# Kernel tuning notes

Measured on AMD Instinct MI355X. Metric: run time of the kernel, lower is better.

The kernel has to match this reference:

```python
import jax, jax.numpy as jnp
import numpy as np

B, S, D, FF, H, N, P, K, KP, R = 2, 512, 256, 1024, 4, 512, 32, 16, 4, 64
DH = D // H  # 64


def _ln(x, g, b):
    mu = x.mean(-1, keepdims=True)
    var = ((x - mu) ** 2).mean(-1, keepdims=True)
    return (x - mu) * jax.lax.rsqrt(var + 1e-5) * g + b


def setup_inputs() -> dict:
    key = jax.random.key(0)
    ks = iter(jax.random.split(key, 40))
    nrm = lambda shape, std=0.02: jax.random.normal(next(ks), shape, jnp.float32) * std
    return dict(
        x=jax.random.normal(next(ks), (B, S, D), jnp.float32),
        g1=jnp.ones((D,), jnp.float32), b1=jnp.zeros((D,), jnp.float32),
        g2=jnp.ones((D,), jnp.float32), b2=jnp.zeros((D,), jnp.float32),
        Wq=nrm((D, D)), bq=jnp.zeros((D,), jnp.float32),
        Wk=nrm((D, D)), bk=jnp.zeros((D,), jnp.float32),
        Wv=nrm((D, D)), bv=jnp.zeros((D,), jnp.float32),
        Wpath=nrm((2 * D, 2)), bpath=jnp.zeros((2,), jnp.float32),
        neurons=nrm((N, D)),
        Wnq=nrm((D, D)), bnq=jnp.zeros((D,), jnp.float32),
        Wnk=nrm((D, D)), bnk=jnp.zeros((D,), jnp.float32),
        Wnv=nrm((D, D)), bnv=jnp.zeros((D,), jnp.float32),
        pattern_queries=nrm((P, D)),
        pattern_up_A=nrm((P, D, R)),
        pattern_up_B=nrm((P, R, FF), 0.01),
        Wub=nrm((D, FF), 0.01), bub=jnp.zeros((FF,), jnp.float32),
        Wd=nrm((FF, D), 0.02), bd=jnp.zeros((D,), jnp.float32),
    )


def _forward(x, g1, b1, g2, b2, Wq, bq, Wk, bk, Wv, bv, Wpath, bpath, neurons,
             Wnq, bnq, Wnk, bnk, Wnv, bnv, pattern_queries, pattern_up_A,
             pattern_up_B, Wub, bub, Wd, bd):
    # ---- NeuronRouter on norm1(x) ----
    n1 = _ln(x, g1, b1)
    q = (n1 @ Wq + bq).reshape(B, S, H, DH)
    k = (n1 @ Wk + bk).reshape(B, S, H, DH)
    v = (n1 @ Wv + bv).reshape(B, S, H, DH)
    attn = jax.nn.softmax(jnp.einsum('bqhd,bkhd->bhqk', q, k) / np.float32(np.sqrt(DH)), axis=-1)
    context = jnp.einsum('bhqk,bkhd->bqhd', attn, v).reshape(B, S, D)
    token_scores = n1 @ neurons.T        # [B,S,N]
    context_scores = context @ neurons.T
    w = jax.nn.softmax(jnp.concatenate([n1, context], -1) @ Wpath + bpath, axis=-1)
    scores = w[..., 0:1] * token_scores + w[..., 1:2] * context_scores
    topk_scores, topk_idx = jax.lax.top_k(scores, K)
    topk_w = jax.nn.softmax(topk_scores, axis=-1)      # [B,S,K]
    selected = neurons[topk_idx]                        # [B,S,K,D]

    # ---- InteractionFFN on norm2(x) ----
    n2 = _ln(x, g2, b2)
    qn = (selected @ Wnq + bnq).reshape(B, S, K, H, DH)
    kn = (selected @ Wnk + bnk).reshape(B, S, K, H, DH)
    vn = jax.nn.sigmoid((selected @ Wnv + bnv).reshape(B, S, K, H, DH))
    aw = jax.nn.softmax(jnp.einsum('bsqhd,bskhd->bshqk', qn, kn) / np.float32(np.sqrt(DH)), axis=-1)
    gates = jnp.einsum('bshqk,bskhd->bsqhd', aw, vn).reshape(B, S, K, D)
    aggregated = jnp.sum(topk_w[..., None] * (selected * gates), axis=2)  # [B,S,D]

    pattern_scores = 0.5 * (aggregated @ pattern_queries.T) / np.float32(np.sqrt(D)) \
                     + 0.5 * (context @ pattern_queries.T)               # [B,S,P]
    tps, tpi = jax.lax.top_k(pattern_scores, KP)
    tpw = jax.nn.softmax(tps, axis=-1)                                   # [B,S,KP]

    combined = n2 + aggregated
    A = pattern_up_A[tpi]    # [B,S,KP,D,R]  (gathered per-token LoRA A)
    Bm = pattern_up_B[tpi]   # [B,S,KP,R,FF] (gathered per-token LoRA B)
    h_mid = jnp.einsum('bsd,bskdr->bskr', combined, A)
    h_pat = jnp.einsum('bskr,bskrf->bskf', h_mid, Bm)
    h_pattern = jnp.sum(tpw[..., None] * h_pat, axis=2)                  # [B,S,FF]
    h = jax.nn.gelu(0.1 * (combined @ Wub + bub) + 0.9 * h_pattern, approximate=False)
    out = h @ Wd + bd
    return x + out, topk_idx


def reference(x, g1, b1, g2, b2, Wq, bq, Wk, bk, Wv, bv, Wpath, bpath, neurons,
              Wnq, bnq, Wnk, bnk, Wnv, bnv, pattern_queries, pattern_up_A,
              pattern_up_B, Wub, bub, Wd, bd):
    return _forward(x, g1, b1, g2, b2, Wq, bq, Wk, bk, Wv, bv, Wpath, bpath,
                    neurons, Wnq, bnq, Wnk, bnk, Wnv, bnv, pattern_queries,
                    pattern_up_A, pattern_up_B, Wub, bub, Wd, bd)
```

## Files before the change

### kernel.cpp

```cpp
#include <hip/hip_runtime.h>
#include <hip/hip_bf16.h>
#include <math.h>

#define BB 2
#define SS 512
#define DD 256
#define FFD 1024
#define HH 4
#define NN 512
#define PP 32
#define KK 16
#define KPP 4
#define RR 64
#define DHH 64
#define TT (BB*SS)
#define QT 16

__global__ __launch_bounds__(256) void ln_kernel(
    const float* __restrict__ x,
    const float* __restrict__ g1, const float* __restrict__ b1,
    const float* __restrict__ g2, const float* __restrict__ b2,
    float* __restrict__ n1, float* __restrict__ n2)
{
    int t = blockIdx.x;
    int d = threadIdx.x;
    __shared__ float red[256];
    float v = x[t*DD + d];
    red[d] = v; __syncthreads();
    for (int s = 128; s > 0; s >>= 1) { if (d < s) red[d] += red[d+s]; __syncthreads(); }
    float mu = red[0] * (1.0f/DD);
    __syncthreads();
    float dv = v - mu;
    red[d] = dv*dv; __syncthreads();
    for (int s = 128; s > 0; s >>= 1) { if (d < s) red[d] += red[d+s]; __syncthreads(); }
    float var = red[0] * (1.0f/DD);
    float r = 1.0f / sqrtf(var + 1e-5f);
    n1[t*DD+d] = dv*r*g1[d] + b1[d];
    n2[t*DD+d] = dv*r*g2[d] + b2[d];
}

__device__ __forceinline__ void gemm_body(
    const float* __restrict__ A, const float* __restrict__ Bm,
    const float* __restrict__ bias, const float* __restrict__ extra,
    float* __restrict__ C, int M, int Nn, int Kk, int transB, int mode,
    int k0off, int kLen)
{
    __shared__ float As[2][32][68];
    __shared__ float Bs[2][32][68];
    int bm = blockIdx.y * 64;
    int bn = blockIdx.x * 64;
    int tid = threadIdx.x;
    int tx = tid & 15, ty = tid >> 4;

    float4 pa[2], pb[2];

    #define LOAD_A(kbase) { \
        _Pragma("unroll") \
        for (int e = 0; e < 2; ++e) { \
            int r = e*32 + (tid>>3); int c4 = tid & 7; \
            pa[e] = *(const float4*)&A[(size_t)(bm + r)*Kk + (kbase) + c4*4]; \
        } }
    #define STORE_A(buf) { \
        _Pragma("unroll") \
        for (int e = 0; e < 2; ++e) { \
            int r = e*32 + (tid>>3); int c4 = tid & 7; \
            As[buf][c4*4+0][r] = pa[e].x; \
            As[buf][c4*4+1][r] = pa[e].y; \
            As[buf][c4*4+2][r] = pa[e].z; \
            As[buf][c4*4+3][r] = pa[e].w; \
        } }
    #define LOAD_B(kbase) { \
        if (transB == 0) { \
            _Pragma("unroll") \
            for (int e = 0; e < 2; ++e) { \
                int c = e*16 + (tid>>4); int n4 = tid & 15; \
                pb[e] = *(const float4*)&Bm[(size_t)((kbase) + c)*Nn + bn + n4*4]; \
            } \
        } else { \
            _Pragma("unroll") \
            for (int e = 0; e < 2; ++e) { \
                int r = e*32 + (tid>>3); int k4 = tid & 7; \
                pb[e] = *(const float4*)&Bm[(size_t)(bn + r)*Kk + (kbase) + k4*4]; \
            } \
        } }
    #define STORE_B(buf) { \
        if (transB == 0) { \
            _Pragma("unroll") \
            for (int e = 0; e < 2; ++e) { \
                int c = e*16 + (tid>>4); int n4 = tid & 15; \
                *(float4*)&Bs[buf][c][n4*4] = pb[e]; \
            } \
        } else { \
            _Pragma("unroll") \
            for (int e = 0; e < 2; ++e) { \
                int r = e*32 + (tid>>3); int k4 = tid & 7; \
                Bs[buf][k4*4+0][r] = pb[e].x; \
                Bs[buf][k4*4+1][r] = pb[e].y; \
                Bs[buf][k4*4+2][r] = pb[e].z; \
                Bs[buf][k4*4+3][r] = pb[e].w; \
            } \
        } }

    float acc[4][4] = {};
    int nk = kLen >> 5;

    LOAD_A(k0off); LOAD_B(k0off);
    STORE_A(0); STORE_B(0);
    __syncthreads();

    for (int kt = 0; kt < nk; ++kt) {
        int cur = kt & 1;
        if (kt + 1 < nk) { LOAD_A(k0off + (kt+1)*32); LOAD_B(k0off + (kt+1)*32); }
        #pragma unroll
        for (int kk = 0; kk < 32; ++kk) {
            float4 av = *(const float4*)&As[cur][kk][ty*4];
            float4 bv = *(const float4*)&Bs[cur][kk][tx*4];
            acc[0][0] = fmaf(av.x, bv.x, acc[0][0]);
            acc[0][1] = fmaf(av.x, bv.y, acc[0][1]);
            acc[0][2] = fmaf(av.x, bv.z, acc[0][2]);
            acc[0][3] = fmaf(av.x, bv.w, acc[0][3]);
            acc[1][0] = fmaf(av.y, bv.x, acc[1][0]);
            acc[1][1] = fmaf(av.y, bv.y, acc[1][1]);
            acc[1][2] = fmaf(av.y, bv.z, acc[1][2]);
            acc[1][3] = fmaf(av.y, bv.w, acc[1][3]);
            acc[2][0] = fmaf(av.z, bv.x, acc[2][0]);
            acc[2][1] = fmaf(av.z, bv.y, acc[2][1]);
            acc[2][2] = fmaf(av.z, bv.z, acc[2][2]);
            acc[2][3] = fmaf(av.z, bv.w, acc[2][3]);
            acc[3][0] = fmaf(av.w, bv.x, acc[3][0]);
            acc[3][1] = fmaf(av.w, bv.y, acc[3][1]);
            acc[3][2] = fmaf(av.w, bv.z, acc[3][2]);
            acc[3][3] = fmaf(av.w, bv.w, acc[3][3]);
        }
        if (kt + 1 < nk) {
            STORE_A(cur^1); STORE_B(cur^1);
            __syncthreads();
        }
    }

    #pragma unroll
    for (int i = 0; i < 4; ++i) {
        int m = bm + ty*4 + i;
        #pragma unroll
        for (int j = 0; j < 4; ++j) {
            int n = bn + tx*4 + j;
            float val = acc[i][j] + (bias ? bias[n] : 0.0f);
            if (mode == 1) {
                val = 1.0f / (1.0f + expf(-val));
            } else if (mode == 2) {
                float z = 0.1f*val + 0.9f*extra[(size_t)m*Nn+n];
                val = 0.5f*z*(1.0f + erff(z*0.70710678118654752f));
            } else if (mode == 3) {
                val = val + extra[(size_t)m*Nn+n];
            }
            C[(size_t)m*Nn + n] = val;
        }
    }
    #undef LOAD_A
    #undef STORE_A
    #undef LOAD_B
    #undef STORE_B
}

__global__ __launch_bounds__(256) void gemm_kernel(
    const float* __restrict__ A, const float* __restrict__ Bm,
    const float* __restrict__ bias, const float* __restrict__ extra,
    float* __restrict__ C, int M, int Nn, int Kk, int transB, int mode)
{
    gemm_body(A, Bm, bias, extra, C, M, Nn, Kk, transB, mode, 0, Kk);
}

struct GemmSet { const float* A; const float* B; const float* bias; float* C; int mode; };

__global__ __launch_bounds__(256) void gemm3_kernel(
    GemmSet s0, GemmSet s1, GemmSet s2, int M, int Nn, int Kk, int transB)
{
    GemmSet s = (blockIdx.z == 0) ? s0 : ((blockIdx.z == 1) ? s1 : s2);
    gemm_body(s.A, s.B, s.bias, nullptr, s.C, M, Nn, Kk, transB, s.mode, 0, Kk);
}

__global__ __launch_bounds__(256) void gemm_splitk_kernel(
    const float* __restrict__ A, const float* __restrict__ Bm,
    float* __restrict__ Cpart, int M, int Nn, int Kk, int kPerSplit)
{
    int sk = blockIdx.z;
    float* Cp = Cpart + (size_t)sk * M * Nn;
    gemm_body(A, Bm, nullptr, nullptr, Cp, M, Nn, Kk, 0, 0, sk*kPerSplit, kPerSplit);
}

__global__ __launch_bounds__(256) void combine_wd_kernel(
    const float* __restrict__ part, const float* __restrict__ x,
    const float* __restrict__ bd, float* __restrict__ out)
{
    int i = blockIdx.x*256 + threadIdx.x;
    int d = i & (DD-1);
    float s = x[i] + bd[d];
    s += part[i] + part[i + TT*DD] + part[i + 2*TT*DD] + part[i + 3*TT*DD];
    out[i] = s;
}

__global__ __launch_bounds__(256) void attn_kernel(
    const float* __restrict__ q, const float* __restrict__ k,
    const float* __restrict__ v, float* __restrict__ ctx)
{
    int bi = blockIdx.x;
    int qt = bi & 31;
    int bh = bi >> 5;
    int h = bh & (HH-1);
    int b = bh >> 2;
    int tid = threadIdx.x;
    int qo = tid >> 4;
    int c  = tid & 15;

    __shared__ float Qs[QT][68];
    __shared__ float Kt[64][64];
    __shared__ float Vs[64][68];
    __shared__ float Ps[QT][68];

    {
        const float* qp = q + ((size_t)(b*SS + qt*QT + qo)*DD) + h*DHH + c*4;
        *(float4*)&Qs[qo][c*4] = *(const float4*)qp;
    }
    float O0=0.f, O1=0.f, O2=0.f, O3=0.f;
    float mreg = -3.4e38f, lreg = 0.f;

    for (int t = 0; t < 8; ++t) {
        if (t) __syncthreads();
        #pragma unroll
        for (int e = 0; e < 4; ++e) {
            int lin = e*256 + tid;
            int kr = lin & 63;
            int c4 = lin >> 6;
            const float* kp = k + ((size_t)(b*SS + t*64 + kr)*DD) + h*DHH + c4*4;
            float4 kv = *(const float4*)kp;
            Kt[c4*4+0][kr] = kv.x;
            Kt[c4*4+1][kr] = kv.y;
            Kt[c4*4+2][kr] = kv.z;
            Kt[c4*4+3][kr] = kv.w;
            int vr = lin >> 4;
            int vc = lin & 15;
            const float* vp = v + ((size_t)(b*SS + t*64 + vr)*DD) + h*DHH + vc*4;
            *(float4*)&Vs[vr][vc*4] = *(const float4*)vp;
        }
        __syncthreads();
        float s0=0.f, s1=0.f, s2=0.f, s3=0.f;
        #pragma unroll 8
        for (int d = 0; d < 64; ++d) {
            float qv = Qs[qo][d];
            float4 kv = *(const float4*)&Kt[d][c*4];
            s0 = fmaf(qv, kv.x, s0);
            s1 = fmaf(qv, kv.y, s1);
            s2 = fmaf(qv, kv.z, s2);
            s3 = fmaf(qv, kv.w, s3);
        }
        s0 *= 0.125f; s1 *= 0.125f; s2 *= 0.125f; s3 *= 0.125f;
        float mx = fmaxf(fmaxf(s0, s1), fmaxf(s2, s3));
        #pragma unroll
        for (int mk = 1; mk <= 8; mk <<= 1)
            mx = fmaxf(mx, __shfl_xor(mx, mk));
        float mnew = fmaxf(mreg, mx);
        float scl = __expf(mreg - mnew);
        float e0 = __expf(s0 - mnew), e1 = __expf(s1 - mnew),
              e2 = __expf(s2 - mnew), e3 = __expf(s3 - mnew);
        float esum = e0 + e1 + e2 + e3;
        #pragma unroll
        for (int mk = 1; mk <= 8; mk <<= 1)
            esum += __shfl_xor(esum, mk);
        lreg = lreg * scl + esum;
        mreg = mnew;
        float4 pw; pw.x = e0; pw.y = e1; pw.z = e2; pw.w = e3;
        *(float4*)&Ps[qo][c*4] = pw;
        __syncthreads();
        O0 *= scl; O1 *= scl; O2 *= scl; O3 *= scl;
        #pragma unroll 8
        for (int kk = 0; kk < 64; ++kk) {
            float pv = Ps[qo][kk];
            float4 vv = *(const float4*)&Vs[kk][c*4];
            O0 = fmaf(pv, vv.x, O0);
            O1 = fmaf(pv, vv.y, O1);
            O2 = fmaf(pv, vv.z, O2);
            O3 = fmaf(pv, vv.w, O3);
        }
    }
    float linv = 1.0f / lreg;
    float4 o4; o4.x = O0*linv; o4.y = O1*linv; o4.z = O2*linv; o4.w = O3*linv;
    *(float4*)(ctx + ((size_t)(b*SS + qt*QT + qo)*DD) + h*DHH + c*4) = o4;
}

__global__ __launch_bounds__(256) void route_kernel(
    const float* __restrict__ n1, const float* __restrict__ ctx,
    const float* __restrict__ Wpath, const float* __restrict__ bpath,
    const float* __restrict__ ts, const float* __restrict__ cs,
    int* __restrict__ topk_idx, float* __restrict__ topk_w,
    float* __restrict__ out_idx)
{
    int t = blockIdx.x, tid = threadIdx.x;
    __shared__ float red0[256], red1[256];
    float a = n1[t*DD+tid], c = ctx[t*DD+tid];
    red0[tid] = a * Wpath[tid*2+0] + c * Wpath[(DD+tid)*2+0];
    red1[tid] = a * Wpath[tid*2+1] + c * Wpath[(DD+tid)*2+1];
    __syncthreads();
    for (int s = 128; s > 0; s >>= 1) {
        if (tid < s) { red0[tid] += red0[tid+s]; red1[tid] += red1[tid+s]; }
        __syncthreads();
    }
    __shared__ float w0s, w1s;
    if (tid == 0) {
        float l0 = red0[0] + bpath[0], l1 = red1[0] + bpath[1];
        float mm = fmaxf(l0, l1);
        float e0 = expf(l0-mm), e1 = expf(l1-mm);
        float is = 1.0f/(e0+e1);
        w0s = e0*is; w1s = e1*is;
    }
    __syncthreads();
    float w0 = w0s, w1 = w1s;
    __shared__ float sc[NN];
    sc[tid]     = w0*ts[t*NN+tid]     + w1*cs[t*NN+tid];
    sc[tid+256] = w0*ts[t*NN+tid+256] + w1*cs[t*NN+tid+256];
    __syncthreads();
    __shared__ float bv_[256]; __shared__ int bi_[256];
    __shared__ float selv[KK]; __shared__ int seli[KK];
    for (int it = 0; it < KK; ++it) {
        float v0 = sc[tid], v1 = sc[tid+256];
        float bv; int bi;
        if (v0 >= v1) { bv = v0; bi = tid; } else { bv = v1; bi = tid+256; }
        bv_[tid] = bv; bi_[tid] = bi;
        __syncthreads();
        for (int s = 128; s > 0; s >>= 1) {
            if (tid < s) {
                float ov = bv_[tid+s]; int oi = bi_[tid+s];
                if (ov > bv_[tid] || (ov == bv_[tid] && oi < bi_[tid])) { bv_[tid] = ov; bi_[tid] = oi; }
            }
            __syncthreads();
        }
        if (tid == 0) { selv[it] = bv_[0]; seli[it] = bi_[0]; sc[bi_[0]] = -3.4e38f; }
        __syncthreads();
    }
    if (tid == 0) {
        float mx = selv[0];
        float e[KK]; float sum = 0.f;
        for (int i = 0; i < KK; ++i) { e[i] = expf(selv[i]-mx); sum += e[i]; }
        float is = 1.0f/sum;
        for (int i = 0; i < KK; ++i) {
            topk_idx[t*KK+i] = seli[i];
            topk_w[t*KK+i]   = e[i]*is;
            out_idx[t*KK+i]  = (float)seli[i];
        }
    }
}

__global__ __launch_bounds__(256) void interact_kernel(
    const float* __restrict__ neurons,
    const float* __restrict__ nqa, const float* __restrict__ nka,
    const float* __restrict__ nva,
    const int* __restrict__ topk_idx, const float* __restrict__ topk_w,
    float* __restrict__ agg)
{
    int t = blockIdx.x, tid = threadIdx.x;
    __shared__ float nq[KK][DD+1];
    __shared__ float nk[KK][DD+1];
    __shared__ float nv[KK][DD+1];
    __shared__ float ps[HH][KK][KK];
    __shared__ float tw[KK];
    __shared__ int sidx[KK];
    if (tid < KK) { tw[tid] = topk_w[t*KK+tid]; sidx[tid] = topk_idx[t*KK+tid]; }
    __syncthreads();
    for (int i = 0; i < KK; ++i) {
        int idx = sidx[i];
        nq[i][tid] = nqa[idx*DD+tid];
        nk[i][tid] = nka[idx*DD+tid];
        nv[i][tid] = nva[idx*DD+tid];
    }
    __syncthreads();
    #pragma unroll
    for (int r = 0; r < 4; ++r) {
        int lin = r*256 + tid;
        int j = lin & 15, i = (lin >> 4) & 15, h = lin >> 8;
        const float* qp = &nq[i][h*DHH];
        const float* kp = &nk[j][h*DHH];
        float acc = 0.f;
        #pragma unroll 8
        for (int d = 0; d < DHH; ++d) acc = fmaf(qp[d], kp[d], acc);
        ps[h][i][j] = acc * 0.125f;
    }
    __syncthreads();
    if (tid < 64) {
        int h = tid >> 4, i = tid & 15;
        float mx = -3.4e38f;
        for (int j = 0; j < KK; ++j) mx = fmaxf(mx, ps[h][i][j]);
        float sum = 0.f;
        for (int j = 0; j < KK; ++j) { float e = expf(ps[h][i][j]-mx); ps[h][i][j] = e; sum += e; }
        float is = 1.0f/sum;
        for (int j = 0; j < KK; ++j) ps[h][i][j] *= is;
    }
    __syncthreads();
    int d = tid, h = d >> 6;
    float acc = 0.f;
    for (int i = 0; i < KK; ++i) {
        float g = 0.f;
        #pragma unroll
        for (int j = 0; j < KK; ++j) g = fmaf(ps[h][i][j], nv[j][d], g);
        acc += tw[i] * neurons[sidx[i]*DD + d] * g;
    }
    agg[t*DD+d] = acc;
}

__global__ __launch_bounds__(256) void pattern_kernel(
    const float* __restrict__ aggp, const float* __restrict__ ctxp,
    const float* __restrict__ n2p, const float* __restrict__ PQ,
    const float* __restrict__ Aup, const float* __restrict__ Bup,
    float* __restrict__ combined, float* __restrict__ hpat)
{
    int t = blockIdx.x, tid = threadIdx.x;
    __shared__ float mix[DD], comb[DD];
    __shared__ float ps[PP];
    __shared__ float psp[8][33];
    __shared__ float hmid[KPP][RR];
    __shared__ int tpi[KPP];
    __shared__ float tpw[KPP];

    float a = aggp[t*DD+tid];
    float cx = ctxp[t*DD+tid];
    mix[tid] = 0.03125f * a + 0.5f * cx;
    float cb = n2p[t*DD+tid] + a;
    comb[tid] = cb;
    combined[t*DD+tid] = cb;
    __syncthreads();

    {
        int p = tid & 31, g = tid >> 5;
        const float* pq = PQ + p*DD + g*32;
        const float* mp = mix + g*32;
        float acc = 0.f;
        #pragma unroll
        for (int d = 0; d < 32; ++d) acc = fmaf(mp[d], pq[d], acc);
        psp[g][p] = acc;
    }
    __syncthreads();
    if (tid < PP) {
        float s = 0.f;
        #pragma unroll
        for (int g = 0; g < 8; ++g) s += psp[g][tid];
        ps[tid] = s;
    }
    __syncthreads();

    if (tid == 0) {
        float vals[KPP];
        #pragma unroll
        for (int it = 0; it < KPP; ++it) {
            float bv = -3.4e38f; int bi = 0;
            for (int p = 0; p < PP; ++p) { float v = ps[p]; if (v > bv) { bv = v; bi = p; } }
            vals[it] = bv; tpi[it] = bi; ps[bi] = -3.4e38f;
        }
        float mx = vals[0];
        float e0 = expf(vals[0]-mx), e1 = expf(vals[1]-mx),
              e2 = expf(vals[2]-mx), e3 = expf(vals[3]-mx);
        float is = 1.0f/(e0+e1+e2+e3);
        tpw[0]=e0*is; tpw[1]=e1*is; tpw[2]=e2*is; tpw[3]=e3*is;
    }
    __syncthreads();

    {
        int kp = tid >> 6, r = tid & 63;
        const float* Ap = Aup + (size_t)tpi[kp]*(DD*RR) + r;
        float acc = 0.f;
        #pragma unroll 8
        for (int d = 0; d < DD; ++d) acc = fmaf(comb[d], Ap[(size_t)d*RR], acc);
        hmid[kp][r] = acc * tpw[kp];
    }
    __syncthreads();

    {
        float4 acc = make_float4(0.f, 0.f, 0.f, 0.f);
        #pragma unroll
        for (int kp = 0; kp < KPP; ++kp) {
            const float4* Bp = (const float4*)(Bup + (size_t)tpi[kp]*(RR*FFD)) + tid;
            const float* hm = hmid[kp];
            #pragma unroll 8
            for (int r = 0; r < RR; ++r) {
                float4 b = Bp[(size_t)r*(FFD/4)];
                float h = hm[r];
                acc.x = fmaf(h, b.x, acc.x);
                acc.y = fmaf(h, b.y, acc.y);
                acc.z = fmaf(h, b.z, acc.z);
                acc.w = fmaf(h, b.w, acc.w);
            }
        }
        ((float4*)(hpat + (size_t)t*FFD))[tid] = acc;
    }
}

extern "C" void kernel_launch(void* const* d_in, const int* in_sizes, int n_in,
                              void* d_out, int out_size, void* d_ws, size_t ws_size,
                              hipStream_t stream)
{
    const float* x        = (const float*)d_in[0];
    const float* g1       = (const float*)d_in[1];
    const float* b1       = (const float*)d_in[2];
    const float* g2       = (const float*)d_in[3];
    const float* b2       = (const float*)d_in[4];
    const float* Wq       = (const float*)d_in[5];
    const float* bq       = (const float*)d_in[6];
    const float* Wk       = (const float*)d_in[7];
    const float* bk       = (const float*)d_in[8];
    const float* Wv       = (const float*)d_in[9];
    const float* bv       = (const float*)d_in[10];
    const float* Wpath    = (const float*)d_in[11];
    const float* bpath    = (const float*)d_in[12];
    const float* neurons  = (const float*)d_in[13];
    const float* Wnq      = (const float*)d_in[14];
    const float* bnq      = (const float*)d_in[15];
    const float* Wnk      = (const float*)d_in[16];
    const float* bnk      = (const float*)d_in[17];
    const float* Wnv      = (const float*)d_in[18];
    const float* bnv      = (const float*)d_in[19];
    const float* PQ       = (const float*)d_in[20];
    const float* Aup      = (const float*)d_in[21];
    const float* Bup      = (const float*)d_in[22];
    const float* Wub      = (const float*)d_in[23];
    const float* bub      = (const float*)d_in[24];
    const float* Wd       = (const float*)d_in[25];
    const float* bd       = (const float*)d_in[26];

    float* out0    = (float*)d_out;
    float* out_idx = out0 + (size_t)TT*DD;

    float* ws = (float*)d_ws;
    float* n1   = ws; ws += TT*DD;
    float* n2   = ws; ws += TT*DD;
    float* qb   = ws; ws += TT*DD;
    float* kb   = ws; ws += TT*DD;
    float* vb   = ws; ws += TT*DD;
    float* ctx  = ws; ws += TT*DD;
    float* ts   = ws; ws += TT*NN;
    float* cs   = ws; ws += TT*NN;
    float* nqa  = ws; ws += NN*DD;
    float* nka  = ws; ws += NN*DD;
    float* nva  = ws; ws += NN*DD;
    float* agg  = ws; ws += TT*DD;
    float* comb = ws; ws += TT*DD;
    float* hpat = ws; ws += TT*FFD;
    float* hb   = ws; ws += TT*FFD;
    float* part = ws; ws += 4*TT*DD;
    float* tkw  = ws; ws += TT*KK;
    int*   tki  = (int*)ws; ws += TT*KK;

    dim3 blk(256);

    ln_kernel<<<TT, blk, 0, stream>>>(x, g1, b1, g2, b2, n1, n2);

    {
        GemmSet sq{n1, Wq, bq, qb, 0}, sk{n1, Wk, bk, kb, 0}, sv{n1, Wv, bv, vb, 0};
        gemm3_kernel<<<dim3(DD/64, TT/64, 3), blk, 0, stream>>>(sq, sk, sv, TT, DD, DD, 0);
    }

    {
        GemmSet s0{neurons, Wnq, bnq, nqa, 0}, s1{neurons, Wnk, bnk, nka, 0},
                s2{neurons, Wnv, bnv, nva, 1};
        gemm3_kernel<<<dim3(DD/64, NN/64, 3), blk, 0, stream>>>(s0, s1, s2, NN, DD, DD, 0);
    }

    attn_kernel<<<BB*HH*(SS/QT), blk, 0, stream>>>(qb, kb, vb, ctx);

    {
        GemmSet s0{n1, neurons, nullptr, ts, 0}, s1{ctx, neurons, nullptr, cs, 0};
        gemm3_kernel<<<dim3(NN/64, TT/64, 2), blk, 0, stream>>>(s0, s1, s1, TT, NN, DD, 1);
    }

    route_kernel<<<TT, blk, 0, stream>>>(n1, ctx, Wpath, bpath, ts, cs, tki, tkw, out_idx);

    interact_kernel<<<TT, blk, 0, stream>>>(neurons, nqa, nka, nva, tki, tkw, agg);

    pattern_kernel<<<TT, blk, 0, stream>>>(agg, ctx, n2, PQ, Aup, Bup, comb, hpat);

    gemm_kernel<<<dim3(FFD/64, TT/64), blk, 0, stream>>>(comb, Wub, bub, hpat, hb, TT, FFD, DD, 0, 2);

    gemm_splitk_kernel<<<dim3(DD/64, TT/64, 4), blk, 0, stream>>>(hb, Wd, part, TT, DD, FFD, FFD/4);
    combine_wd_kernel<<<TT*DD/256, blk, 0, stream>>>(part, x, bd, out0);
}
```

Measured before the change: 318.9 us.

## Bin tokens by selected pattern to reuse LoRA weights across tokens

```diff
diff --git a/kernel.cpp b/kernel.cpp
--- a/kernel.cpp
+++ b/kernel.cpp
@@ -15,6 +15,12 @@
 #define DHH 64
 #define TT (BB*SS)
 #define QT 16
+
+__global__ __launch_bounds__(64) void zero_kernel(int* __restrict__ p, int n)
+{
+    int i = threadIdx.x;
+    if (i < n) p[i] = 0;
+}
 
 __global__ __launch_bounds__(256) void ln_kernel(
     const float* __restrict__ x,
@@ -148,7 +154,10 @@
             if (mode == 1) {
                 val = 1.0f / (1.0f + expf(-val));
             } else if (mode == 2) {
-                float z = 0.1f*val + 0.9f*extra[(size_t)m*Nn+n];
+                size_t idx = (size_t)m*Nn + n;
+                float hp = extra[idx] + extra[idx + (size_t)TT*FFD]
+                         + extra[idx + 2*(size_t)TT*FFD] + extra[idx + 3*(size_t)TT*FFD];
+                float z = 0.1f*val + 0.9f*hp;
                 val = 0.5f*z*(1.0f + erff(z*0.70710678118654752f));
             } else if (mode == 3) {
                 val = val + extra[(size_t)m*Nn+n];
@@ -295,18 +304,22 @@
     float* __restrict__ out_idx)
 {
     int t = blockIdx.x, tid = threadIdx.x;
-    __shared__ float red0[256], red1[256];
+    int wv = tid >> 6;
+    __shared__ float pw0[4], pw1[4];
     float a = n1[t*DD+tid], c = ctx[t*DD+tid];
-    red0[tid] = a * Wpath[tid*2+0] + c * Wpath[(DD+tid)*2+0];
-    red1[tid] = a * Wpath[tid*2+1] + c * Wpath[(DD+tid)*2+1];
-    __syncthreads();
-    for (int s = 128; s > 0; s >>= 1) {
-        if (tid < s) { red0[tid] += red0[tid+s]; red1[tid] += red1[tid+s]; }
-        __syncthreads();
-    }
+    float r0 = a * Wpath[tid*2+0] + c * Wpath[(DD+tid)*2+0];
+    float r1 = a * Wpath[tid*2+1] + c * Wpath[(DD+tid)*2+1];
+    #pragma unroll
+    for (int off = 1; off < 64; off <<= 1) {
+        r0 += __shfl_xor(r0, off);
+        r1 += __shfl_xor(r1, off);
+    }
+    if ((tid & 63) == 0) { pw0[wv] = r0; pw1[wv] = r1; }
+    __syncthreads();
     __shared__ float w0s, w1s;
     if (tid == 0) {
-        float l0 = red0[0] + bpath[0], l1 = red1[0] + bpath[1];
+        float l0 = pw0[0]+pw0[1]+pw0[2]+pw0[3] + bpath[0];
+        float l1 = pw1[0]+pw1[1]+pw1[2]+pw1[3] + bpath[1];
         float mm = fmaxf(l0, l1);
         float e0 = expf(l0-mm), e1 = expf(l1-mm);
         float is = 1.0f/(e0+e1);
@@ -318,22 +331,29 @@
     sc[tid]     = w0*ts[t*NN+tid]     + w1*cs[t*NN+tid];
     sc[tid+256] = w0*ts[t*NN+tid+256] + w1*cs[t*NN+tid+256];
     __syncthreads();
-    __shared__ float bv_[256]; __shared__ int bi_[256];
+    __shared__ float wvv[4]; __shared__ int wvi[4];
     __shared__ float selv[KK]; __shared__ int seli[KK];
     for (int it = 0; it < KK; ++it) {
         float v0 = sc[tid], v1 = sc[tid+256];
         float bv; int bi;
         if (v0 >= v1) { bv = v0; bi = tid; } else { bv = v1; bi = tid+256; }
-        bv_[tid] = bv; bi_[tid] = bi;
+        #pragma unroll
+        for (int off = 1; off < 64; off <<= 1) {
+            float ov = __shfl_xor(bv, off);
+            int   oi = __shfl_xor(bi, off);
+            if (ov > bv || (ov == bv && oi < bi)) { bv = ov; bi = oi; }
+        }
+        if ((tid & 63) == 0) { wvv[wv] = bv; wvi[wv] = bi; }
         __syncthreads();
-        for (int s = 128; s > 0; s >>= 1) {
-            if (tid < s) {
-                float ov = bv_[tid+s]; int oi = bi_[tid+s];
-                if (ov > bv_[tid] || (ov == bv_[tid] && oi < bi_[tid])) { bv_[tid] = ov; bi_[tid] = oi; }
+        if (tid == 0) {
+            float fv = wvv[0]; int fi = wvi[0];
+            #pragma unroll
+            for (int w = 1; w < 4; ++w) {
+                float ov = wvv[w]; int oi = wvi[w];
+                if (ov > fv || (ov == fv && oi < fi)) { fv = ov; fi = oi; }
             }
-            __syncthreads();
-        }
-        if (tid == 0) { selv[it] = bv_[0]; seli[it] = bi_[0]; sc[bi_[0]] = -3.4e38f; }
+            selv[it] = fv; seli[it] = fi; sc[fi] = -3.4e38f;
+        }
         __syncthreads();
     }
     if (tid == 0) {
@@ -405,26 +425,22 @@
     agg[t*DD+d] = acc;
 }
 
-__global__ __launch_bounds__(256) void pattern_kernel(
+__global__ __launch_bounds__(256) void pattern_select(
     const float* __restrict__ aggp, const float* __restrict__ ctxp,
     const float* __restrict__ n2p, const float* __restrict__ PQ,
-    const float* __restrict__ Aup, const float* __restrict__ Bup,
-    float* __restrict__ combined, float* __restrict__ hpat)
+    float* __restrict__ combined, float* __restrict__ tpwg,
+    int* __restrict__ bin_count, int* __restrict__ bin_entry)
 {
     int t = blockIdx.x, tid = threadIdx.x;
-    __shared__ float mix[DD], comb[DD];
+    __shared__ float mix[DD];
     __shared__ float ps[PP];
     __shared__ float psp[8][33];
-    __shared__ float hmid[KPP][RR];
     __shared__ int tpi[KPP];
-    __shared__ float tpw[KPP];
 
     float a = aggp[t*DD+tid];
     float cx = ctxp[t*DD+tid];
     mix[tid] = 0.03125f * a + 0.5f * cx;
-    float cb = n2p[t*DD+tid] + a;
-    comb[tid] = cb;
-    combined[t*DD+tid] = cb;
+    combined[t*DD+tid] = n2p[t*DD+tid] + a;
     __syncthreads();
 
     {
@@ -457,37 +473,92 @@
         float e0 = expf(vals[0]-mx), e1 = expf(vals[1]-mx),
               e2 = expf(vals[2]-mx), e3 = expf(vals[3]-mx);
         float is = 1.0f/(e0+e1+e2+e3);
-        tpw[0]=e0*is; tpw[1]=e1*is; tpw[2]=e2*is; tpw[3]=e3*is;
+        tpwg[t*4+0]=e0*is; tpwg[t*4+1]=e1*is; tpwg[t*4+2]=e2*is; tpwg[t*4+3]=e3*is;
+    }
+    __syncthreads();
+    if (tid < KPP) {
+        int p = tpi[tid];
+        int slot = atomicAdd(&bin_count[p], 1);
+        bin_entry[p*TT + slot] = (t << 2) | tid;
+    }
+}
+
+__global__ __launch_bounds__(256) void pattern_apply(
+    const float* __restrict__ comb, const float* __restrict__ tpwg,
+    const int* __restrict__ bin_count, const int* __restrict__ bin_entry,
+    const float* __restrict__ Aup, const float* __restrict__ Bup,
+    float* __restrict__ hpat4)
+{
+    int p = blockIdx.y, cch = blockIdx.x;
+    int cnt = bin_count[p];
+    int base = cch * 16;
+    if (base >= cnt) return;
+    int nt = cnt - base; if (nt > 16) nt = 16;
+    int tid = threadIdx.x;
+
+    __shared__ int toks[16]; __shared__ int kps[16]; __shared__ float wts[16];
+    __shared__ float combs[16][DD+1];
+    __shared__ float hmid[16][RR];
+
+    if (tid < 16) {
+        if (tid < nt) {
+            int e = bin_entry[p*TT + base + tid];
+            int t = e >> 2, kp = e & 3;
+            toks[tid] = t; kps[tid] = kp; wts[tid] = tpwg[t*4 + kp];
+        } else { toks[tid] = -1; wts[tid] = 0.f; }
+    }
+    __syncthreads();
+    #pragma unroll
+    for (int i = 0; i < 16; ++i) {
+        int t = toks[i];
+        combs[i][tid] = (t >= 0) ? comb[(size_t)t*DD + tid] : 0.f;
     }
     __syncthreads();
 
     {
-        int kp = tid >> 6, r = tid & 63;
-        const float* Ap = Aup + (size_t)tpi[kp]*(DD*RR) + r;
-        float acc = 0.f;
+        int i = tid >> 4, g = tid & 15;
+        const float* Ap = Aup + (size_t)p*(DD*RR) + g*4;
+        float a0=0.f, a1=0.f, a2=0.f, a3=0.f;
         #pragma unroll 8
-        for (int d = 0; d < DD; ++d) acc = fmaf(comb[d], Ap[(size_t)d*RR], acc);
-        hmid[kp][r] = acc * tpw[kp];
-    }
-    __syncthreads();
-
-    {
-        float4 acc = make_float4(0.f, 0.f, 0.f, 0.f);
-        #pragma unroll
-        for (int kp = 0; kp < KPP; ++kp) {
-            const float4* Bp = (const float4*)(Bup + (size_t)tpi[kp]*(RR*FFD)) + tid;
-            const float* hm = hmid[kp];
-            #pragma unroll 8
-            for (int r = 0; r < RR; ++r) {
-                float4 b = Bp[(size_t)r*(FFD/4)];
-                float h = hm[r];
-                acc.x = fmaf(h, b.x, acc.x);
-                acc.y = fmaf(h, b.y, acc.y);
-                acc.z = fmaf(h, b.z, acc.z);
-                acc.w = fmaf(h, b.w, acc.w);
-            }
-        }
-        ((float4*)(hpat + (size_t)t*FFD))[tid] = acc;
+        for (int d = 0; d < DD; ++d) {
+            float cv = combs[i][d];
+            float4 av = *(const float4*)&Ap[(size_t)d*RR];
+            a0 = fmaf(cv, av.x, a0);
+            a1 = fmaf(cv, av.y, a1);
+            a2 = fmaf(cv, av.z, a2);
+            a3 = fmaf(cv, av.w, a3);
+        }
+        float w = wts[i];
+        hmid[i][g*4+0] = a0*w;
+        hmid[i][g*4+1] = a1*w;
+        hmid[i][g*4+2] = a2*w;
+        hmid[i][g*4+3] = a3*w;
+    }
+    __syncthreads();
+
+    float4 acc[16];
+    #pragma unroll
+    for (int i = 0; i < 16; ++i) acc[i] = make_float4(0.f,0.f,0.f,0.f);
+    const float* Bp = Bup + (size_t)p*(RR*FFD) + tid*4;
+    for (int r4 = 0; r4 < RR/4; ++r4) {
+        float4 b0 = *(const float4*)&Bp[(size_t)(r4*4+0)*FFD];
+        float4 b1 = *(const float4*)&Bp[(size_t)(r4*4+1)*FFD];
+        float4 b2 = *(const float4*)&Bp[(size_t)(r4*4+2)*FFD];
+        float4 b3 = *(const float4*)&Bp[(size_t)(r4*4+3)*FFD];
+        #pragma unroll
+        for (int i = 0; i < 16; ++i) {
+            float4 h = *(const float4*)&hmid[i][r4*4];
+            acc[i].x = fmaf(h.x,b0.x, fmaf(h.y,b1.x, fmaf(h.z,b2.x, fmaf(h.w,b3.x, acc[i].x))));
+            acc[i].y = fmaf(h.x,b0.y, fmaf(h.y,b1.y, fmaf(h.z,b2.y, fmaf(h.w,b3.y, acc[i].y))));
+            acc[i].z = fmaf(h.x,b0.z, fmaf(h.y,b1.z, fmaf(h.z,b2.z, fmaf(h.w,b3.z, acc[i].z))));
+            acc[i].w = fmaf(h.x,b0.w, fmaf(h.y,b1.w, fmaf(h.z,b2.w, fmaf(h.w,b3.w, acc[i].w))));
+        }
+    }
+    #pragma unroll
+    for (int i = 0; i < 16; ++i) {
+        int t = toks[i];
+        if (t >= 0)
+            *(float4*)&hpat4[(size_t)kps[i]*(TT*FFD) + (size_t)t*FFD + tid*4] = acc[i];
     }
 }
 
@@ -527,26 +598,31 @@
     float* out_idx = out0 + (size_t)TT*DD;
 
     float* ws = (float*)d_ws;
-    float* n1   = ws; ws += TT*DD;
-    float* n2   = ws; ws += TT*DD;
-    float* qb   = ws; ws += TT*DD;
-    float* kb   = ws; ws += TT*DD;
-    float* vb   = ws; ws += TT*DD;
-    float* ctx  = ws; ws += TT*DD;
-    float* ts   = ws; ws += TT*NN;
-    float* cs   = ws; ws += TT*NN;
-    float* nqa  = ws; ws += NN*DD;
-    float* nka  = ws; ws += NN*DD;
-    float* nva  = ws; ws += NN*DD;
-    float* agg  = ws; ws += TT*DD;
-    float* comb = ws; ws += TT*DD;
-    float* hpat = ws; ws += TT*FFD;
-    float* hb   = ws; ws += TT*FFD;
-    float* part = ws; ws += 4*TT*DD;
-    float* tkw  = ws; ws += TT*KK;
-    int*   tki  = (int*)ws; ws += TT*KK;
+    float* n1    = ws; ws += TT*DD;
+    float* n2    = ws; ws += TT*DD;
+    float* qb    = ws; ws += TT*DD;
+    float* kb    = ws; ws += TT*DD;
+    float* vb    = ws; ws += TT*DD;
+    float* ctx   = ws; ws += TT*DD;
+    float* ts    = ws; ws += TT*NN;
+    float* cs    = ws; ws += TT*NN;
+    float* nqa   = ws; ws += NN*DD;
+    float* nka   = ws; ws += NN*DD;
+    float* nva   = ws; ws += NN*DD;
+    float* agg   = ws; ws += TT*DD;
+    float* comb  = ws; ws += TT*DD;
+    float* hpat4 = ws; ws += 4*TT*FFD;
+    float* hb    = ws; ws += TT*FFD;
+    float* part  = ws; ws += 4*TT*DD;
+    float* tkw   = ws; ws += TT*KK;
+    float* tpwg  = ws; ws += TT*KPP;
+    int*   tki   = (int*)ws; ws += TT*KK;
+    int*   binc  = (int*)ws; ws += 32;
+    int*   bine  = (int*)ws; ws += 32*TT;
 
     dim3 blk(256);
+
+    zero_kernel<<<1, 64, 0, stream>>>(binc, 32);
 
     ln_kernel<<<TT, blk, 0, stream>>>(x, g1, b1, g2, b2, n1, n2);
 
@@ -572,9 +648,11 @@
 
     interact_kernel<<<TT, blk, 0, stream>>>(neurons, nqa, nka, nva, tki, tkw, agg);
 
-    pattern_kernel<<<TT, blk, 0, stream>>>(agg, ctx, n2, PQ, Aup, Bup, comb, hpat);
-
-    gemm_kernel<<<dim3(FFD/64, TT/64), blk, 0, stream>>>(comb, Wub, bub, hpat, hb, TT, FFD, DD, 0, 2);
+    pattern_select<<<TT, blk, 0, stream>>>(agg, ctx, n2, PQ, comb, tpwg, binc, bine);
+
+    pattern_apply<<<dim3(TT/16, PP), blk, 0, stream>>>(comb, tpwg, binc, bine, Aup, Bup, hpat4);
+
+    gemm_kernel<<<dim3(FFD/64, TT/64), blk, 0, stream>>>(comb, Wub, bub, hpat4, hb, TT, FFD, DD, 0, 2);
 
     gemm_splitk_kernel<<<dim3(DD/64, TT/64, 4), blk, 0, stream>>>(hb, Wd, part, TT, DD, FFD, FFD/4);
     combine_wd_kernel<<<TT*DD/256, blk, 0, stream>>>(part, x, bd, out0);
```

New measurement: 342.3 us. 7.4% more time.
